# Kernel tuning notes

Hardware: AMD Instinct MI355X
Metric: run time of the kernel (lower is better)

Reference implementation:

```python
import jax, jax.numpy as jnp
import numpy as np

BN_EPS = 1e-5
KEEP_RATIO = 0.25
MIN_TOPK = 4


def setup_inputs() -> dict:
    key = jax.random.key(0)
    ks = jax.random.split(key, 8)
    B, C, H, W, HID = 32, 768, 32, 32, 96
    x = jax.random.normal(ks[0], (B, C, H, W), dtype=jnp.float32)
    # fan-in scaled weights so score magnitudes stay sane for softmax
    w1 = jax.random.normal(ks[1], (HID, C, 1, 1), dtype=jnp.float32) / np.sqrt(C)
    bn_gamma = jax.random.uniform(ks[2], (HID,), dtype=jnp.float32) + 0.5
    bn_beta = jax.random.normal(ks[3], (HID,), dtype=jnp.float32) * 0.1
    bn_mean = jax.random.normal(ks[4], (HID,), dtype=jnp.float32) * 0.1
    bn_var = jax.random.uniform(ks[5], (HID,), dtype=jnp.float32) + 0.5
    w2 = jax.random.normal(ks[6], (1, HID, 3, 3), dtype=jnp.float32) / np.sqrt(HID * 9)
    b2 = jax.random.normal(ks[7], (1,), dtype=jnp.float32) * 0.1
    return {"x": x, "w1": w1, "bn_gamma": bn_gamma, "bn_beta": bn_beta,
            "bn_mean": bn_mean, "bn_var": bn_var, "w2": w2, "b2": b2}


def reference(x, w1, bn_gamma, bn_beta, bn_mean, bn_var, w2, b2):
    B, C, H, W = x.shape
    N = H * W
    # 1x1 conv (no bias) as channel contraction: [B,C,H,W] x [HID,C] -> [B,HID,H,W]
    h = jnp.einsum('bchw,oc->bohw', x, w1[:, :, 0, 0])
    # BatchNorm in inference mode (running stats)
    scale = (bn_gamma / jnp.sqrt(bn_var + BN_EPS))[None, :, None, None]
    h = h * scale + (bn_beta - bn_mean * bn_gamma / jnp.sqrt(bn_var + BN_EPS))[None, :, None, None]
    h = jax.nn.relu(h)
    # 3x3 conv HID -> 1, padding=1
    score = jax.lax.conv_general_dilated(
        h, w2, window_strides=(1, 1), padding='SAME',
        dimension_numbers=('NCHW', 'OIHW', 'NCHW')) + b2[None, :, None, None]
    s = score.reshape(B, N)
    K = min(max(MIN_TOPK, int(N * KEEP_RATIO)), N)
    top_vals, top_idx = jax.lax.top_k(s, K)  # [B,K] (sorted; weighted sum is order-invariant)
    x_flat = x.reshape(B, C, N)
    sel = jnp.take_along_axis(x_flat, top_idx[:, None, :], axis=2)  # [B,C,K]
    w = jax.nn.softmax(top_vals, axis=1)[:, None, :]               # [B,1,K]
    v = jnp.sum(sel * w, axis=2)                                    # [B,C]
    # dropout p=0.0 -> identity
    return v, score.reshape(B, 1, H, W)
```

## Files before the change

kernel.cpp:

```cpp
#include <hip/hip_runtime.h>
#include <math.h>

#define BB 32
#define CC 768
#define HID 96
#define NPIX 1024
#define KSEL 256
#define BN_EPS_F 1e-5f

typedef __bf16 bf16x8 __attribute__((ext_vector_type(8)));
typedef float f32x4 __attribute__((ext_vector_type(4)));

__device__ __forceinline__ unsigned short f2bf(float f) {
    unsigned u = __float_as_uint(f);
    return (unsigned short)((u + 0x7FFFu + ((u >> 16) & 1u)) >> 16);
}
__device__ __forceinline__ unsigned pack2(float lo, float hi) {
    return (unsigned)f2bf(lo) | ((unsigned)f2bf(hi) << 16);
}

__global__ __launch_bounds__(256) void k0_prep(
    const float* __restrict__ w1, const float* __restrict__ gamma,
    const float* __restrict__ beta, const float* __restrict__ mean,
    const float* __restrict__ var,
    unsigned short* __restrict__ w1b, float* __restrict__ scale,
    float* __restrict__ shift)
{
    int t = threadIdx.x, bk = blockIdx.x;
    if (bk < 72) {
        int idx = (bk * 256 + t) * 4;
        float4 v = *reinterpret_cast<const float4*>(w1 + idx);
        uint2 o;
        o.x = pack2(v.x, v.y);
        o.y = pack2(v.z, v.w);
        *reinterpret_cast<uint2*>(w1b + idx) = o;
    } else if (t < HID) {
        float sc = gamma[t] * rsqrtf(var[t] + BN_EPS_F);
        scale[t] = sc;
        shift[t] = beta[t] - mean[t] * sc;
    }
}

__global__ __launch_bounds__(256) void k1_gemm_mfma(
    const float* __restrict__ x, const unsigned short* __restrict__ w1b,
    const float* __restrict__ scale, const float* __restrict__ shift,
    float* __restrict__ h_out)
{
    __shared__ unsigned Xs[2][32][132];
    __shared__ unsigned short W1s[2][96][72];
    __shared__ float sc_s[HID], sh_s[HID];

    const int t = threadIdx.x;
    const int b = blockIdx.y;
    const int n0 = blockIdx.x * 128;
    const int wave = t >> 6, lane = t & 63;
    const int lm = lane & 15, g = lane >> 4;
    const int kp = t >> 3, q = t & 7;

    if (t < HID) { sc_s[t] = scale[t]; sh_s[t] = shift[t]; }

    f32x4 acc[6][2];
#pragma unroll
    for (int mt = 0; mt < 6; ++mt)
#pragma unroll
        for (int ns = 0; ns < 2; ++ns) acc[mt][ns] = (f32x4){0.f, 0.f, 0.f, 0.f};

    const float* xbase = x + (size_t)b * CC * NPIX + n0;

    {
        const float* r0 = xbase + (size_t)(2 * kp) * NPIX;
        const float* r1 = r0 + NPIX;
#pragma unroll
        for (int j = 0; j < 4; ++j) {
            int nc = q * 16 + 4 * j;
            float4 a4 = *reinterpret_cast<const float4*>(r0 + nc);
            float4 b4 = *reinterpret_cast<const float4*>(r1 + nc);
            uint4 pk;
            pk.x = pack2(a4.x, b4.x); pk.y = pack2(a4.y, b4.y);
            pk.z = pack2(a4.z, b4.z); pk.w = pack2(a4.w, b4.w);
            *reinterpret_cast<uint4*>(&Xs[0][kp][nc]) = pk;
        }
#pragma unroll
        for (int i = 0; i < 3; ++i) {
            int idx = t + i * 256;
            int m = idx >> 3, ko = (idx & 7) * 8;
            uint4 wv = *reinterpret_cast<const uint4*>(w1b + (size_t)m * CC + ko);
            *reinterpret_cast<uint4*>(&W1s[0][m][ko]) = wv;
        }
    }
    __syncthreads();

    int cur = 0;
    for (int c0 = 0; c0 < CC; c0 += 64) {
        const bool hasNext = (c0 + 64 < CC);
        float4 xa[4], xb[4];
        uint4 wreg[3];
        if (hasNext) {
            const float* r0 = xbase + (size_t)(c0 + 64 + 2 * kp) * NPIX;
            const float* r1 = r0 + NPIX;
#pragma unroll
            for (int j = 0; j < 4; ++j) {
                int nc = q * 16 + 4 * j;
                xa[j] = *reinterpret_cast<const float4*>(r0 + nc);
                xb[j] = *reinterpret_cast<const float4*>(r1 + nc);
            }
#pragma unroll
            for (int i = 0; i < 3; ++i) {
                int idx = t + i * 256;
                int m = idx >> 3, ko = (idx & 7) * 8;
                wreg[i] = *reinterpret_cast<const uint4*>(
                    w1b + (size_t)m * CC + c0 + 64 + ko);
            }
        }
#pragma unroll
        for (int half = 0; half < 2; ++half) {
            uint4 au[6];
#pragma unroll
            for (int mt = 0; mt < 6; ++mt)
                au[mt] = *reinterpret_cast<const uint4*>(
                    &W1s[cur][mt * 16 + lm][half * 32 + g * 8]);
#pragma unroll
            for (int ns = 0; ns < 2; ++ns) {
                int nl = wave * 32 + ns * 16 + lm;
                uint4 bu;
                bu.x = Xs[cur][16 * half + 4 * g + 0][nl];
                bu.y = Xs[cur][16 * half + 4 * g + 1][nl];
                bu.z = Xs[cur][16 * half + 4 * g + 2][nl];
                bu.w = Xs[cur][16 * half + 4 * g + 3][nl];
                bf16x8 bfr = __builtin_bit_cast(bf16x8, bu);
#pragma unroll
                for (int mt = 0; mt < 6; ++mt)
                    acc[mt][ns] = __builtin_amdgcn_mfma_f32_16x16x32_bf16(
                        __builtin_bit_cast(bf16x8, au[mt]), bfr, acc[mt][ns], 0, 0, 0);
            }
        }
        if (hasNext) {
#pragma unroll
            for (int j = 0; j < 4; ++j) {
                int nc = q * 16 + 4 * j;
                uint4 pk;
                pk.x = pack2(xa[j].x, xb[j].x); pk.y = pack2(xa[j].y, xb[j].y);
                pk.z = pack2(xa[j].z, xb[j].z); pk.w = pack2(xa[j].w, xb[j].w);
                *reinterpret_cast<uint4*>(&Xs[cur ^ 1][kp][nc]) = pk;
            }
#pragma unroll
            for (int i = 0; i < 3; ++i) {
                int idx = t + i * 256;
                int m = idx >> 3, ko = (idx & 7) * 8;
                *reinterpret_cast<uint4*>(&W1s[cur ^ 1][m][ko]) = wreg[i];
            }
        }
        __syncthreads();
        cur ^= 1;
    }

#pragma unroll
    for (int mt = 0; mt < 6; ++mt)
#pragma unroll
        for (int ns = 0; ns < 2; ++ns) {
#pragma unroll
            for (int r = 0; r < 4; ++r) {
                int o = mt * 16 + g * 4 + r;
                int n = n0 + wave * 32 + ns * 16 + lm;
                float v = fmaxf(acc[mt][ns][r] * sc_s[o] + sh_s[o], 0.f);
                h_out[((size_t)b * HID + o) * NPIX + n] = v;
            }
        }
}

__global__ __launch_bounds__(128) void k2_conv3x3(
    const float* __restrict__ h_in, const float* __restrict__ w2,
    const float* __restrict__ b2, float* __restrict__ score_out)
{
    __shared__ float hs[16][6][40];
    __shared__ float w2s[HID * 9];

    const int t = threadIdx.x;
    const int ytile = blockIdx.x, b = blockIdx.y;
    const int y = t >> 5, xx = t & 31;
    const int Y = ytile * 4 + y;

    for (int i = t; i < HID * 9; i += 128) w2s[i] = w2[i];

    const float* hb = h_in + (size_t)b * HID * NPIX;
    float acc = 0.f;

    for (int c0 = 0; c0 < HID; c0 += 16) {
        __syncthreads();
        for (int i = t; i < 192; i += 128) {
            int ch = i / 12, rr = (i % 12) >> 1, col = (i & 1) ? 36 : 3;
            hs[ch][rr][col] = 0.f;
        }
#pragma unroll
        for (int i = 0; i < 6; ++i) {
            int idx = t + i * 128;
            int ch = idx / 48, rem = idx % 48;
            int rr = rem >> 3, qq = rem & 7;
            int gy = ytile * 4 - 1 + rr;
            float4 v = (gy >= 0 && gy < 32)
                ? *reinterpret_cast<const float4*>(
                      hb + (size_t)(c0 + ch) * NPIX + gy * 32 + qq * 4)
                : (float4){0.f, 0.f, 0.f, 0.f};
            *reinterpret_cast<float4*>(&hs[ch][rr][4 + qq * 4]) = v;
        }
        __syncthreads();
#pragma unroll
        for (int ch = 0; ch < 16; ++ch) {
            float s = 0.f;
#pragma unroll
            for (int ky = 0; ky < 3; ++ky)
#pragma unroll
                for (int kx = 0; kx < 3; ++kx)
                    s += hs[ch][y + ky][3 + xx + kx] * w2s[(c0 + ch) * 9 + ky * 3 + kx];
            acc += s;
        }
    }
    score_out[b * NPIX + Y * 32 + xx] = acc + b2[0];
}

__global__ __launch_bounds__(256) void k3_topk_softmax(
    const float* __restrict__ score, float* __restrict__ weight)
{
    __shared__ unsigned hist[256];
    __shared__ unsigned wtot[4];
    __shared__ unsigned pcnt16[16];
    __shared__ float redf[4];
    __shared__ unsigned sh_bin, sh_rem;

    const int t = threadIdx.x, b = blockIdx.x;
    const int lane = t & 63, wv = t >> 6;

    float fvals[4];
    unsigned uvals[4];
#pragma unroll
    for (int i = 0; i < 4; ++i) {
        float f = score[b * NPIX + t + 256 * i];
        fvals[i] = f;
        unsigned u = __float_as_uint(f);
        uvals[i] = (u & 0x80000000u) ? ~u : (u | 0x80000000u);
    }

    unsigned prefix = 0, rem = KSEL;
    for (int p = 3; p >= 0; --p) {
        hist[t] = 0;
        __syncthreads();
        const int sh_hi = (p + 1) * 8;
#pragma unroll
        for (int i = 0; i < 4; ++i) {
            unsigned u = uvals[i];
            bool match = (p == 3) || ((u >> sh_hi) == (prefix >> sh_hi));
            if (match) atomicAdd(&hist[(u >> (p * 8)) & 0xffu], 1u);
        }
        __syncthreads();
        unsigned own = hist[t];
        unsigned val = own;
#pragma unroll
        for (int off = 1; off <= 32; off <<= 1) {
            unsigned o2 = __shfl_down(val, off);
            if (lane + off < 64) val += o2;
        }
        if (lane == 0) wtot[wv] = val;
        __syncthreads();
        unsigned suff = val;
        for (int w = wv + 1; w < 4; ++w) suff += wtot[w];
        unsigned nexts = suff - own;
        if (suff >= rem && nexts < rem) { sh_bin = (unsigned)t; sh_rem = rem - nexts; }
        __syncthreads();
        prefix |= (sh_bin << (p * 8));
        rem = sh_rem;
        __syncthreads();
    }
    const unsigned T = prefix, need = rem;

    float m = -INFINITY;
#pragma unroll
    for (int i = 0; i < 4; ++i) m = fmaxf(m, fvals[i]);
#pragma unroll
    for (int off = 32; off >= 1; off >>= 1) m = fmaxf(m, __shfl_xor(m, off));
    if (lane == 0) redf[wv] = m;
    __syncthreads();
    m = fmaxf(fmaxf(redf[0], redf[1]), fmaxf(redf[2], redf[3]));

    unsigned lp[4]; bool eqf[4], gtf[4];
    unsigned long long lmask = (1ULL << lane) - 1ULL;
#pragma unroll
    for (int i = 0; i < 4; ++i) {
        bool eq = (uvals[i] == T);
        eqf[i] = eq; gtf[i] = (uvals[i] > T);
        unsigned long long mk = __ballot(eq);
        lp[i] = (unsigned)__popcll(mk & lmask);
        if (lane == 0) pcnt16[i * 4 + wv] = (unsigned)__popcll(mk);
    }
    __syncthreads();
    unsigned cum = 0, baseArr[4];
#pragma unroll
    for (int ii = 0; ii < 4; ++ii) {
        unsigned b0 = cum;
        for (int w = 0; w < wv; ++w) b0 += pcnt16[ii * 4 + w];
        baseArr[ii] = b0;
        for (int w = 0; w < 4; ++w) cum += pcnt16[ii * 4 + w];
    }
    float evals[4], sumExp = 0.f;
#pragma unroll
    for (int i = 0; i < 4; ++i) {
        bool sel = gtf[i] || (eqf[i] && (baseArr[i] + lp[i]) < need);
        float e = sel ? expf(fvals[i] - m) : 0.f;
        evals[i] = e;
        sumExp += e;
    }
#pragma unroll
    for (int off = 32; off >= 1; off >>= 1) sumExp += __shfl_xor(sumExp, off);
    if (lane == 0) redf[wv] = sumExp;
    __syncthreads();
    float inv = 1.0f / (redf[0] + redf[1] + redf[2] + redf[3]);
#pragma unroll
    for (int i = 0; i < 4; ++i)
        weight[b * NPIX + i * 256 + t] = evals[i] * inv;
}

__global__ __launch_bounds__(256) void k4_weighted_sum(
    const float* __restrict__ x, const float* __restrict__ weight,
    float* __restrict__ v)
{
    __shared__ float wsm[NPIX];
    const int t = threadIdx.x;
    const int b = blockIdx.x / 192, cg = blockIdx.x % 192;

    *reinterpret_cast<float4*>(&wsm[t * 4]) =
        *reinterpret_cast<const float4*>(&weight[b * NPIX + t * 4]);
    __syncthreads();

    const int lane = t & 63, wvv = t >> 6;
    const int c = cg * 4 + wvv;
    const float* xr = x + ((size_t)b * CC + c) * NPIX;

    float acc = 0.f;
#pragma unroll
    for (int j = 0; j < 4; ++j) {
        int off = j * 256 + lane * 4;
        float4 xv = *reinterpret_cast<const float4*>(xr + off);
        float4 wv4 = *reinterpret_cast<const float4*>(&wsm[off]);
        acc += xv.x * wv4.x + xv.y * wv4.y + xv.z * wv4.z + xv.w * wv4.w;
    }
#pragma unroll
    for (int off = 32; off >= 1; off >>= 1) acc += __shfl_xor(acc, off);
    if (lane == 0) v[(size_t)b * CC + c] = acc;
}

extern "C" void kernel_launch(void* const* d_in, const int* in_sizes, int n_in,
                              void* d_out, int out_size, void* d_ws, size_t ws_size,
                              hipStream_t stream)
{
    const float* x     = (const float*)d_in[0];
    const float* w1    = (const float*)d_in[1];
    const float* gamma = (const float*)d_in[2];
    const float* beta  = (const float*)d_in[3];
    const float* mean  = (const float*)d_in[4];
    const float* var   = (const float*)d_in[5];
    const float* w2    = (const float*)d_in[6];
    const float* b2    = (const float*)d_in[7];

    float* out   = (float*)d_out;
    float* vout  = out;
    float* score = out + BB * CC;

    float* h       = (float*)d_ws;
    float* weight  = h + (size_t)BB * HID * NPIX;
    unsigned short* w1b = (unsigned short*)(weight + BB * NPIX);
    float* scale   = (float*)(w1b + HID * CC);
    float* shift   = scale + HID;

    k0_prep<<<73, 256, 0, stream>>>(w1, gamma, beta, mean, var, w1b, scale, shift);
    k1_gemm_mfma<<<dim3(8, BB), 256, 0, stream>>>(x, w1b, scale, shift, h);
    k2_conv3x3<<<dim3(8, BB), 128, 0, stream>>>(h, w2, b2, score);
    k3_topk_softmax<<<BB, 256, 0, stream>>>(score, weight);
    k4_weighted_sum<<<BB * (CC / 4), 256, 0, stream>>>(x, weight, vout);
}
```

Baseline: 91.26 us.

## Retile 1x1-conv GEMM to 64-pixel blocks and stream weights through registers

The GEMM kernel now uses 512-thread blocks covering 64 pixels instead of 256-thread blocks covering 128. Each wave handles 48 output channels by 16 pixels. The W1 tile is no longer staged in shared memory: each lane loads its bf16 weight fragments straight from global memory into registers, double-buffered across two K-chunks, and only X stays in a shared double buffer. The aim is twice as many blocks for better CU occupancy and less LDS traffic, at the cost of redundant global weight loads, which should mostly hit cache, and more barriers per K step.

New measurement: 95.95 us. 1.05x slower.

```diff
diff --git a/kernel.cpp b/kernel.cpp
--- a/kernel.cpp
+++ b/kernel.cpp
@@ -41,131 +41,131 @@
     }
 }
 
-__global__ __launch_bounds__(256) void k1_gemm_mfma(
+__global__ __launch_bounds__(512, 4) void k1_gemm_mfma(
     const float* __restrict__ x, const unsigned short* __restrict__ w1b,
     const float* __restrict__ scale, const float* __restrict__ shift,
     float* __restrict__ h_out)
 {
-    __shared__ unsigned Xs[2][32][132];
-    __shared__ unsigned short W1s[2][96][72];
+    __shared__ unsigned Xs[2][32][66];
     __shared__ float sc_s[HID], sh_s[HID];
 
     const int t = threadIdx.x;
     const int b = blockIdx.y;
-    const int n0 = blockIdx.x * 128;
+    const int n0 = blockIdx.x * 64;
     const int wave = t >> 6, lane = t & 63;
     const int lm = lane & 15, g = lane >> 4;
-    const int kp = t >> 3, q = t & 7;
+    const int wo = wave >> 2, wn = wave & 3;
+    const int nB = wn * 16 + lm;
+    const int kp = t >> 4, q = t & 15;
+    const int nc = q * 4;
 
     if (t < HID) { sc_s[t] = scale[t]; sh_s[t] = shift[t]; }
 
-    f32x4 acc[6][2];
-#pragma unroll
-    for (int mt = 0; mt < 6; ++mt)
-#pragma unroll
-        for (int ns = 0; ns < 2; ++ns) acc[mt][ns] = (f32x4){0.f, 0.f, 0.f, 0.f};
+    f32x4 acc[3];
+#pragma unroll
+    for (int mt = 0; mt < 3; ++mt) acc[mt] = (f32x4){0.f, 0.f, 0.f, 0.f};
 
     const float* xbase = x + (size_t)b * CC * NPIX + n0;
+    const unsigned short* wrow = w1b + (size_t)(wo * 48 + lm) * CC;
+
+    uint4 wA[6], wB[6];
 
     {
         const float* r0 = xbase + (size_t)(2 * kp) * NPIX;
-        const float* r1 = r0 + NPIX;
-#pragma unroll
-        for (int j = 0; j < 4; ++j) {
-            int nc = q * 16 + 4 * j;
+        float4 a4 = *reinterpret_cast<const float4*>(r0 + nc);
+        float4 b4 = *reinterpret_cast<const float4*>(r0 + NPIX + nc);
+        uint4 pk;
+        pk.x = pack2(a4.x, b4.x); pk.y = pack2(a4.y, b4.y);
+        pk.z = pack2(a4.z, b4.z); pk.w = pack2(a4.w, b4.w);
+        *reinterpret_cast<uint4*>(&Xs[0][kp][nc]) = pk;
+#pragma unroll
+        for (int mt = 0; mt < 3; ++mt)
+#pragma unroll
+            for (int h = 0; h < 2; ++h)
+                wA[mt * 2 + h] = *reinterpret_cast<const uint4*>(
+                    wrow + (size_t)mt * 16 * CC + h * 32 + g * 8);
+    }
+    __syncthreads();
+
+#pragma unroll 1
+    for (int j = 0; j < 6; ++j) {
+        const int cA = 2 * j * 64;
+        const int cB = cA + 64;
+        {
+            const float* r0 = xbase + (size_t)(cB + 2 * kp) * NPIX;
             float4 a4 = *reinterpret_cast<const float4*>(r0 + nc);
-            float4 b4 = *reinterpret_cast<const float4*>(r1 + nc);
+            float4 b4 = *reinterpret_cast<const float4*>(r0 + NPIX + nc);
+#pragma unroll
+            for (int mt = 0; mt < 3; ++mt)
+#pragma unroll
+                for (int h = 0; h < 2; ++h)
+                    wB[mt * 2 + h] = *reinterpret_cast<const uint4*>(
+                        wrow + (size_t)mt * 16 * CC + cB + h * 32 + g * 8);
+#pragma unroll
+            for (int h = 0; h < 2; ++h) {
+                uint4 bu;
+                bu.x = Xs[0][16 * h + 4 * g + 0][nB];
+                bu.y = Xs[0][16 * h + 4 * g + 1][nB];
+                bu.z = Xs[0][16 * h + 4 * g + 2][nB];
+                bu.w = Xs[0][16 * h + 4 * g + 3][nB];
+                bf16x8 bfr = __builtin_bit_cast(bf16x8, bu);
+#pragma unroll
+                for (int mt = 0; mt < 3; ++mt)
+                    acc[mt] = __builtin_amdgcn_mfma_f32_16x16x32_bf16(
+                        __builtin_bit_cast(bf16x8, wA[mt * 2 + h]), bfr, acc[mt], 0, 0, 0);
+            }
             uint4 pk;
             pk.x = pack2(a4.x, b4.x); pk.y = pack2(a4.y, b4.y);
             pk.z = pack2(a4.z, b4.z); pk.w = pack2(a4.w, b4.w);
-            *reinterpret_cast<uint4*>(&Xs[0][kp][nc]) = pk;
-        }
-#pragma unroll
-        for (int i = 0; i < 3; ++i) {
-            int idx = t + i * 256;
-            int m = idx >> 3, ko = (idx & 7) * 8;
-            uint4 wv = *reinterpret_cast<const uint4*>(w1b + (size_t)m * CC + ko);
-            *reinterpret_cast<uint4*>(&W1s[0][m][ko]) = wv;
-        }
-    }
-    __syncthreads();
-
-    int cur = 0;
-    for (int c0 = 0; c0 < CC; c0 += 64) {
-        const bool hasNext = (c0 + 64 < CC);
-        float4 xa[4], xb[4];
-        uint4 wreg[3];
-        if (hasNext) {
-            const float* r0 = xbase + (size_t)(c0 + 64 + 2 * kp) * NPIX;
-            const float* r1 = r0 + NPIX;
-#pragma unroll
-            for (int j = 0; j < 4; ++j) {
-                int nc = q * 16 + 4 * j;
-                xa[j] = *reinterpret_cast<const float4*>(r0 + nc);
-                xb[j] = *reinterpret_cast<const float4*>(r1 + nc);
+            *reinterpret_cast<uint4*>(&Xs[1][kp][nc]) = pk;
+        }
+        __syncthreads();
+        {
+            const bool hasNext = (j < 5);
+            float4 a4, b4;
+            if (hasNext) {
+                const float* r0 = xbase + (size_t)(cB + 64 + 2 * kp) * NPIX;
+                a4 = *reinterpret_cast<const float4*>(r0 + nc);
+                b4 = *reinterpret_cast<const float4*>(r0 + NPIX + nc);
+#pragma unroll
+                for (int mt = 0; mt < 3; ++mt)
+#pragma unroll
+                    for (int h = 0; h < 2; ++h)
+                        wA[mt * 2 + h] = *reinterpret_cast<const uint4*>(
+                            wrow + (size_t)mt * 16 * CC + cB + 64 + h * 32 + g * 8);
             }
 #pragma unroll
-            for (int i = 0; i < 3; ++i) {
-                int idx = t + i * 256;
-                int m = idx >> 3, ko = (idx & 7) * 8;
-                wreg[i] = *reinterpret_cast<const uint4*>(
-                    w1b + (size_t)m * CC + c0 + 64 + ko);
+            for (int h = 0; h < 2; ++h) {
+                uint4 bu;
+                bu.x = Xs[1][16 * h + 4 * g + 0][nB];
+                bu.y = Xs[1][16 * h + 4 * g + 1][nB];
+                bu.z = Xs[1][16 * h + 4 * g + 2][nB];
+                bu.w = Xs[1][16 * h + 4 * g + 3][nB];
+                bf16x8 bfr = __builtin_bit_cast(bf16x8, bu);
+#pragma unroll
+                for (int mt = 0; mt < 3; ++mt)
+                    acc[mt] = __builtin_amdgcn_mfma_f32_16x16x32_bf16(
+                        __builtin_bit_cast(bf16x8, wB[mt * 2 + h]), bfr, acc[mt], 0, 0, 0);
             }
-        }
-#pragma unroll
-        for (int half = 0; half < 2; ++half) {
-            uint4 au[6];
-#pragma unroll
-            for (int mt = 0; mt < 6; ++mt)
-                au[mt] = *reinterpret_cast<const uint4*>(
-                    &W1s[cur][mt * 16 + lm][half * 32 + g * 8]);
-#pragma unroll
-            for (int ns = 0; ns < 2; ++ns) {
-                int nl = wave * 32 + ns * 16 + lm;
-                uint4 bu;
-                bu.x = Xs[cur][16 * half + 4 * g + 0][nl];
-                bu.y = Xs[cur][16 * half + 4 * g + 1][nl];
-                bu.z = Xs[cur][16 * half + 4 * g + 2][nl];
-                bu.w = Xs[cur][16 * half + 4 * g + 3][nl];
-                bf16x8 bfr = __builtin_bit_cast(bf16x8, bu);
-#pragma unroll
-                for (int mt = 0; mt < 6; ++mt)
-                    acc[mt][ns] = __builtin_amdgcn_mfma_f32_16x16x32_bf16(
-                        __builtin_bit_cast(bf16x8, au[mt]), bfr, acc[mt][ns], 0, 0, 0);
+            if (hasNext) {
+                uint4 pk;
+                pk.x = pack2(a4.x, b4.x); pk.y = pack2(a4.y, b4.y);
+                pk.z = pack2(a4.z, b4.z); pk.w = pack2(a4.w, b4.w);
+                *reinterpret_cast<uint4*>(&Xs[0][kp][nc]) = pk;
+                __syncthreads();
             }
         }
-        if (hasNext) {
-#pragma unroll
-            for (int j = 0; j < 4; ++j) {
-                int nc = q * 16 + 4 * j;
-                uint4 pk;
-                pk.x = pack2(xa[j].x, xb[j].x); pk.y = pack2(xa[j].y, xb[j].y);
-                pk.z = pack2(xa[j].z, xb[j].z); pk.w = pack2(xa[j].w, xb[j].w);
-                *reinterpret_cast<uint4*>(&Xs[cur ^ 1][kp][nc]) = pk;
-            }
-#pragma unroll
-            for (int i = 0; i < 3; ++i) {
-                int idx = t + i * 256;
-                int m = idx >> 3, ko = (idx & 7) * 8;
-                *reinterpret_cast<uint4*>(&W1s[cur ^ 1][m][ko]) = wreg[i];
-            }
-        }
-        __syncthreads();
-        cur ^= 1;
-    }
-
-#pragma unroll
-    for (int mt = 0; mt < 6; ++mt)
-#pragma unroll
-        for (int ns = 0; ns < 2; ++ns) {
-#pragma unroll
-            for (int r = 0; r < 4; ++r) {
-                int o = mt * 16 + g * 4 + r;
-                int n = n0 + wave * 32 + ns * 16 + lm;
-                float v = fmaxf(acc[mt][ns][r] * sc_s[o] + sh_s[o], 0.f);
-                h_out[((size_t)b * HID + o) * NPIX + n] = v;
-            }
-        }
+    }
+
+#pragma unroll
+    for (int mt = 0; mt < 3; ++mt) {
+#pragma unroll
+        for (int r = 0; r < 4; ++r) {
+            int o = wo * 48 + mt * 16 + g * 4 + r;
+            float v = fmaxf(acc[mt][r] * sc_s[o] + sh_s[o], 0.f);
+            h_out[((size_t)b * HID + o) * NPIX + n0 + nB] = v;
+        }
+    }
 }
 
 __global__ __launch_bounds__(128) void k2_conv3x3(
@@ -371,7 +371,7 @@
     float* shift   = scale + HID;
 
     k0_prep<<<73, 256, 0, stream>>>(w1, gamma, beta, mean, var, w1b, scale, shift);
-    k1_gemm_mfma<<<dim3(8, BB), 256, 0, stream>>>(x, w1b, scale, shift, h);
+    k1_gemm_mfma<<<dim3(16, BB), 512, 0, stream>>>(x, w1b, scale, shift, h);
     k2_conv3x3<<<dim3(8, BB), 128, 0, stream>>>(h, w2, b2, score);
     k3_topk_softmax<<<BB, 256, 0, stream>>>(score, weight);
     k4_weighted_sum<<<BB * (CC / 4), 256, 0, stream>>>(x, weight, vout);
```
